# Kernel optimization log

Measured on AMD Instinct MI355X. Metric: run time of the kernel, lower is better.

The kernel has to match this reference:

```python
import jax, jax.numpy as jnp
import numpy as np

N_NODES = 16000
N_EDGES = 256000
F = 128        # invariant edge feature dim
MUL = 64       # multiplicity of env/V irreps (mul_gcd)
HID = 128      # mlp_n_hidden
SQRT3 = float(np.sqrt(3.0))

# e3nn-style activation normalization constant for silu:
# c = sqrt(E_{z~N(0,1)}[silu(z)^2]), so silu(z)/c has unit second moment.
_z = np.linspace(-12.0, 12.0, 100001)
_pdf = np.exp(-0.5 * _z ** 2) / np.sqrt(2.0 * np.pi)
_silu = _z / (1.0 + np.exp(-_z))
SILU_C = float(np.sqrt(np.trapz(_silu ** 2 * _pdf, _z)))


def _nsilu(x):
    return jax.nn.silu(x) / SILU_C


def _lin(x, W):
    # e3nn 'path' gradient normalization: W ~ N(0,1), forward scaled by 1/sqrt(fan_in)
    return (x @ W) / jnp.sqrt(jnp.asarray(W.shape[0], x.dtype))


def setup_inputs() -> dict:
    key = jax.random.key(0)
    ks = jax.random.split(key, 11)
    inp = {
        'vectors': jax.random.normal(ks[0], (N_EDGES, 3), jnp.float32),
        'x': jax.random.normal(ks[1], (N_EDGES, F), jnp.float32),
        'V': jax.random.normal(ks[2], (N_EDGES, 4 * MUL), jnp.float32),  # 64x0e + 64x1o
        'u': jax.random.uniform(ks[3], (N_EDGES,), jnp.float32),
        'm': jnp.ones((N_EDGES,), jnp.float32),
        'W_env': jax.random.normal(ks[4], (F, 2 * MUL), jnp.float32),
        'W1': jax.random.normal(ks[5], (F + 2 * MUL, HID), jnp.float32),
        'W2': jax.random.normal(ks[6], (HID, HID), jnp.float32),
        'W3': jax.random.normal(ks[7], (HID, HID), jnp.float32),
        'W_out': jax.random.normal(ks[8], (2 * MUL, MUL), jnp.float32),
        'senders': jax.random.randint(ks[9], (N_EDGES,), 0, N_NODES, jnp.int32),
    }
    return inp


def reference(vectors, x, V, u, m, W_env, W1, W2, W3, W_out, senders):
    E = vectors.shape[0]
    x = x * m[:, None]

    # n_neighbors = scatter_sum(m, dst=senders, map_back=True)
    n_neighbors = jax.ops.segment_sum(m, senders, num_segments=N_NODES)[senders]  # (E,)

    # w = Linear(num_irreps=2*MUL)(x)
    w = _lin(x, W_env)                  # (E, 128)
    w0, w1 = w[:, :MUL], w[:, MUL:]     # scalar / vector channel weights

    # spherical harmonics (component normalization): Y0 = 1, Y1 = sqrt(3)*rhat
    rhat = vectors / jnp.linalg.norm(vectors, axis=-1, keepdims=True)
    Y1 = SQRT3 * rhat                   # (E, 3)

    # w * Y * m, scatter_sum over senders, map back, normalize by n_neighbors
    denom = n_neighbors + 1e-5
    ws = w0 * m[:, None]                                   # (E, MUL)   w * Y0
    wv = (w1[:, :, None] * Y1[:, None, :]) * m[:, None, None]  # (E, MUL, 3)
    wY_s = jax.ops.segment_sum(ws, senders, num_segments=N_NODES)[senders] / denom[:, None]
    wY_v = jax.ops.segment_sum(wv, senders, num_segments=N_NODES)[senders] / denom[:, None, None]

    # V.mul_to_axis(): (E, MUL, 0e+1o)
    Vs = V[:, :MUL]                      # (E, MUL)
    Vv = V[:, MUL:].reshape(E, MUL, 3)   # (E, MUL, 3)

    # tensor product, filter_ir_out = {0e, 1o} (CG, component normalization)
    s_a = wY_s * Vs                                  # 0e x 0e -> 0e
    s_b = jnp.sum(wY_v * Vv, axis=-1) / SQRT3        # 1o x 1o -> 0e
    v_a = wY_s[:, :, None] * Vv                      # 0e x 1o -> 1o
    v_b = wY_v * Vs[:, :, None]                      # 1o x 0e -> 1o

    # scalars -> concatenated into x; vectors stay equivariant
    x = jnp.concatenate([x, s_a, s_b], axis=1)       # (E, F + 2*MUL)

    # invariant MLP (silu, no output activation)
    h = _nsilu(_lin(x, W1))
    h = _nsilu(_lin(h, W2))
    h = _lin(h, W3)                                  # (E, HID)
    x_out = u[:, None] * h

    # Linear(irreps_out=64x1o) on 128x1o
    V_in = jnp.concatenate([v_a, v_b], axis=1)       # (E, 2*MUL, 3)
    V_out = jnp.einsum('euk,uo->eok', V_in, W_out) / jnp.sqrt(jnp.asarray(2 * MUL, V.dtype))
    V_out = V_out.reshape(E, MUL * 3)                # (E, 192)

    return x_out, V_out
```

## Files before the change

### kernel.cpp

```cpp
#include <hip/hip_runtime.h>
#include <math.h>

typedef short bf16x8 __attribute__((ext_vector_type(8)));
typedef float f32x4 __attribute__((ext_vector_type(4)));

#define S128 0.08838834764831845f
#define S256I 0.0625f
#define NN_NODES 16000

#define WS_COUNTS   16448000
#define WS_OFFSETS  (WS_COUNTS + 64000)
#define WS_CURSOR   (WS_OFFSETS + 64000)
#define WS_INV      (WS_CURSOR + 64000)
#define WS_W1 (WS_INV + 1024000)
#define WS_W2 (WS_W1 + 65536)
#define WS_W3 (WS_W2 + 32768)
#define WS_WO (WS_W3 + 32768)
#define WS_WE (WS_WO + 16384)
#define WS_VECM (WS_WE + 32768)
#define WS_XMB  (WS_VECM + 4096000)

static float compute_inv_silu_c() {
    double sum = 0.0, prev = 0.0;
    const double dz = 24.0 / 100000.0;
    for (int i = 0; i <= 100000; ++i) {
        double z = -12.0 + dz * (double)i;
        double pdf = exp(-0.5 * z * z) * 0.3989422804014327;
        double s = z / (1.0 + exp(-z));
        double f = s * s * pdf;
        if (i) sum += 0.5 * (prev + f) * dz;
        prev = f;
    }
    return (float)(1.0 / sqrt(sum));
}
static const float INV_SILU_C = compute_inv_silu_c();

__device__ __forceinline__ unsigned int packbf(float a, float b) {
    union { float f; unsigned int u; } ca, cb;
    ca.f = a; cb.f = b;
    unsigned int ua = ca.u + (0x7fffu + ((ca.u >> 16) & 1u));
    unsigned int ub = cb.u + (0x7fffu + ((cb.u >> 16) & 1u));
    return (ua >> 16) | (ub & 0xffff0000u);
}
__device__ __forceinline__ unsigned short bf16r(float v) {
    union { float f; unsigned int u; } c; c.f = v;
    return (unsigned short)((c.u + (0x7fffu + ((c.u >> 16) & 1u))) >> 16);
}
__device__ __forceinline__ float bflo(unsigned int u) { return __uint_as_float(u << 16); }
__device__ __forceinline__ float bfhi(unsigned int u) { return __uint_as_float(u & 0xffff0000u); }
__device__ __forceinline__ int swz(int row, int b) { return b ^ ((row & 7) << 4); }
__device__ __forceinline__ float nsilu(float v, float ic) {
    return v / (1.0f + __expf(-v)) * ic;
}

__global__ __launch_bounds__(256) void k_wprep(
    const float* __restrict__ W1, const float* __restrict__ W2,
    const float* __restrict__ W3, const float* __restrict__ Wout,
    const float* __restrict__ Wenv, char* __restrict__ wsb)
{
    const int t = blockIdx.x * 256 + threadIdx.x;
    if (t < NN_NODES) ((int*)(wsb + WS_COUNTS))[t] = 0;
    if (t < 32768) {
        int n = t & 127, k = t >> 7;
        *(unsigned short*)(wsb + WS_W1 + n * 512 + k * 2) =
            bf16r(W1[k * 128 + n] * S256I);
    }
    if (t < 16384) {
        int n = t & 127, k = t >> 7;
        *(unsigned short*)(wsb + WS_W2 + n * 256 + k * 2) =
            bf16r(W2[k * 128 + n] * S128);
        *(unsigned short*)(wsb + WS_W3 + n * 256 + k * 2) =
            bf16r(W3[k * 128 + n] * S128);
    }
    if (t < 16384) {
        int j = t & 127, k = t >> 7;
        int c = (j & 1) ? 64 + (j >> 1) : (j >> 1);
        *(unsigned short*)(wsb + WS_WE + j * 256 + k * 2) =
            bf16r(Wenv[k * 128 + c] * S128);
    }
    if (t < 8192) {
        int o = t & 63, uu = t >> 6;
        *(unsigned short*)(wsb + WS_WO + o * 256 + ((uu * 2) ^ ((o & 7) << 4))) =
            bf16r(Wout[uu * 64 + o] * S128);
    }
}

__global__ __launch_bounds__(1024) void k_hist(
    const int* __restrict__ senders, int* __restrict__ counts, int E)
{
    const int e = blockIdx.x * 1024 + threadIdx.x;
    if (e < E) atomicAdd(&counts[senders[e]], 1);
}

__global__ __launch_bounds__(1024) void k_scan(
    const int* __restrict__ counts, int* __restrict__ offsets,
    int* __restrict__ cursor)
{
    __shared__ int part[1024];
    const int t = threadIdx.x;
    const int s0 = t * 16;
    const int s1 = (s0 + 16 < NN_NODES) ? s0 + 16 : NN_NODES;
    int s = 0;
    for (int i = s0; i < s1; ++i) s += counts[i];
    part[t] = s;
    __syncthreads();
    for (int off = 1; off < 1024; off <<= 1) {
        int v = part[t];
        if (t >= off) v += part[t - off];
        __syncthreads();
        part[t] = v;
        __syncthreads();
    }
    int run = t ? part[t - 1] : 0;
    for (int i = s0; i < s1; ++i) {
        offsets[i] = run; cursor[i] = run; run += counts[i];
    }
}

__global__ __launch_bounds__(1024) void k_binfill(
    const int* __restrict__ senders, const float* __restrict__ vectors,
    const float* __restrict__ m, int* __restrict__ cursor,
    int* __restrict__ inv, float4* __restrict__ vecm, int E)
{
    const int e = blockIdx.x * 1024 + threadIdx.x;
    if (e < E) {
        const int p = atomicAdd(&cursor[senders[e]], 1);
        inv[e] = p;
        float4 vm;
        vm.x = vectors[(size_t)e * 3 + 0];
        vm.y = vectors[(size_t)e * 3 + 1];
        vm.z = vectors[(size_t)e * 3 + 2];
        vm.w = m[e];
        vecm[p] = vm;
    }
}

__global__ __launch_bounds__(512) void k_env(
    const float* __restrict__ x, const float* __restrict__ m,
    const char* __restrict__ wsb, const int* __restrict__ inv,
    char* __restrict__ wout, char* __restrict__ xmb, int E)
{
    __shared__ char lds[32768];
    const int tid = threadIdx.x, l = tid & 63, wid = tid >> 6;
    const int lr = l & 15, lg = l >> 4;
    const int n0 = wid * 16;

    bf16x8 B[4];
    #pragma unroll
    for (int kk = 0; kk < 4; ++kk)
        B[kk] = *(const bf16x8*)(wsb + WS_WE + (n0 + lr) * 256 + kk * 64 + lg * 16);

    const int eb = blockIdx.x * 128;
    {
        const int el = tid >> 2, q = tid & 3;
        const int e = eb + el;
        if (e < E) {
            const float mv = m[e];
            const float4* xp = (const float4*)&x[(size_t)e * 128 + q * 32];
            #pragma unroll
            for (int j = 0; j < 4; ++j) {
                float4 A = xp[2 * j], Bv = xp[2 * j + 1];
                int4 w;
                w.x = packbf(A.x * mv, A.y * mv); w.y = packbf(A.z * mv, A.w * mv);
                w.z = packbf(Bv.x * mv, Bv.y * mv); w.w = packbf(Bv.z * mv, Bv.w * mv);
                *(int4*)(lds + el * 256 + swz(el, q * 64 + j * 16)) = w;
            }
        } else {
            const int4 z = {0, 0, 0, 0};
            #pragma unroll
            for (int j = 0; j < 4; ++j)
                *(int4*)(lds + el * 256 + swz(el, q * 64 + j * 16)) = z;
        }
    }
    __syncthreads();

    {
        const int el = tid >> 2, q = tid & 3;
        const int e = eb + el;
        if (e < E) {
            int4* d = (int4*)(xmb + (size_t)e * 256 + q * 64);
            #pragma unroll
            for (int j = 0; j < 4; ++j)
                d[j] = *(int4*)(lds + el * 256 + ((q * 64 + j * 16) ^ ((el & 7) << 4)));
        }
    }

    f32x4 acc[8];
    #pragma unroll
    for (int a = 0; a < 8; ++a) acc[a] = (f32x4){0.f, 0.f, 0.f, 0.f};

    #pragma unroll
    for (int kk = 0; kk < 4; ++kk) {
        const int kb = kk * 64 + lg * 16;
        #pragma unroll
        for (int mt = 0; mt < 8; ++mt) {
            const int row = mt * 16 + lr;
            bf16x8 a = *(const bf16x8*)(lds + row * 256 + swz(row, kb));
            acc[mt] = __builtin_amdgcn_mfma_f32_16x16x32_bf16(a, B[kk], acc[mt], 0, 0, 0);
        }
    }
    __syncthreads();

    #pragma unroll
    for (int mt = 0; mt < 8; ++mt)
        #pragma unroll
        for (int r = 0; r < 4; ++r) {
            const int row = mt * 16 + lg * 4 + r;
            *(unsigned short*)(lds + row * 256 + (((n0 + lr) * 2) ^ ((row & 7) << 4))) =
                bf16r(acc[mt][r]);
        }
    __syncthreads();

    {
        const int el = tid >> 2, q = tid & 3;
        const int e = eb + el;
        if (e < E) {
            const int p = inv[e];
            int4* d = (int4*)(wout + (size_t)p * 256 + q * 64);
            #pragma unroll
            for (int j = 0; j < 4; ++j)
                d[j] = *(int4*)(lds + el * 256 + ((q * 64 + j * 16) ^ ((el & 7) << 4)));
        }
    }
}

__global__ __launch_bounds__(256) void k_gather(
    const char* __restrict__ wvb, const float4* __restrict__ vecm,
    const int* __restrict__ counts, const int* __restrict__ offsets,
    float* __restrict__ node_cnt, float* __restrict__ node_s,
    float* __restrict__ node_v)
{
    const int l = threadIdx.x & 63, wid = threadIdx.x >> 6;
    const int n = blockIdx.x * 4 + wid;
    if (n >= NN_NODES) return;
    const int cnt = counts[n], base = offsets[n];

    float as = 0.f, a0 = 0.f, a1 = 0.f, a2 = 0.f, am = 0.f;
    for (int i = 0; i < cnt; ++i) {
        const unsigned int wv =
            *(const unsigned int*)(wvb + (size_t)(base + i) * 256 + l * 4);
        const float4 vm = vecm[base + i];
        const float rn = 1.7320508075688772f /
                         sqrtf(vm.x * vm.x + vm.y * vm.y + vm.z * vm.z);
        const float w0 = bflo(wv) * vm.w;
        const float c1 = bfhi(wv) * vm.w * rn;
        as += w0; am += vm.w;
        a0 += c1 * vm.x; a1 += c1 * vm.y; a2 += c1 * vm.z;
    }
    if (l == 0) node_cnt[n] = am;
    node_s[(size_t)n * 64 + l] = as;
    float* nv = &node_v[((size_t)n * 64 + l) * 3];
    nv[0] = a0; nv[1] = a1; nv[2] = a2;
}

__global__ __launch_bounds__(512, 4) void k_fuse(
    const float* __restrict__ V, const int* __restrict__ senders,
    const float* __restrict__ node_cnt, const float* __restrict__ node_s,
    const float* __restrict__ node_v, const char* __restrict__ wsb,
    const char* __restrict__ xmb, const float* __restrict__ ug,
    float* __restrict__ out_x, float* __restrict__ out_v,
    float inv_c, int E)
{
    __shared__ char lds[81920];
    const int tid = threadIdx.x, l = tid & 63, wid = tid >> 6;
    const int lr = l & 15, lg = l >> 4;

    {
        const int4* src = (const int4*)(wsb + WS_WO);
        ((int4*)(lds + 49152))[tid * 2]     = src[tid * 2];
        ((int4*)(lds + 49152))[tid * 2 + 1] = src[tid * 2 + 1];
    }

    const int eb = blockIdx.x * 64;
    #pragma unroll 2
    for (int i = 0; i < 8; ++i) {
        const int el = wid * 8 + i;
        const int e  = eb + el;
        float Vs = 0.f, Vv0 = 0.f, Vv1 = 0.f, Vv2 = 0.f;
        float wYs = 0.f, wv0 = 0.f, wv1 = 0.f, wv2 = 0.f;
        if (e < E) {
            Vs = V[(size_t)e * 256 + l];
            const float* vp = &V[(size_t)e * 256 + 64 + l * 3];
            Vv0 = vp[0]; Vv1 = vp[1]; Vv2 = vp[2];
            const int sn = senders[e];
            const float rden = 1.0f / (node_cnt[sn] + 1e-5f);
            wYs = node_s[(size_t)sn * 64 + l] * rden;
            const float* nvp = &node_v[((size_t)sn * 64 + l) * 3];
            wv0 = nvp[0] * rden; wv1 = nvp[1] * rden; wv2 = nvp[2] * rden;
        }
        *(unsigned short*)(lds + 65536 + el * 256 + l * 2) = bf16r(wYs * Vs);
        *(unsigned short*)(lds + 65536 + el * 256 + 128 + l * 2) =
            bf16r((wv0 * Vv0 + wv1 * Vv1 + wv2 * Vv2) * 0.57735026918962576f);
        const float vvk[3] = {Vv0, Vv1, Vv2};
        const float wvk[3] = {wv0, wv1, wv2};
        #pragma unroll
        for (int k = 0; k < 3; ++k) {
            const int row = el * 3 + k;
            *(unsigned short*)(lds + row * 256 + swz(row, l * 2))       = bf16r(wYs * vvk[k]);
            *(unsigned short*)(lds + row * 256 + swz(row, 128 + l * 2)) = bf16r(wvk[k] * Vs);
        }
    }
    __syncthreads();

    {
        const int wm = wid & 3, wn = wid >> 2;
        const int m0 = wm * 48, n0v = wn * 32;
        f32x4 acc[3][2];
        #pragma unroll
        for (int a = 0; a < 3; ++a)
            #pragma unroll
            for (int b = 0; b < 2; ++b) acc[a][b] = (f32x4){0.f, 0.f, 0.f, 0.f};

        #pragma unroll
        for (int kk = 0; kk < 4; ++kk) {
            const int kb = kk * 64 + lg * 16;
            bf16x8 a0 = *(const bf16x8*)(lds + (m0 + lr) * 256      + swz(m0 + lr, kb));
            bf16x8 a1 = *(const bf16x8*)(lds + (m0 + 16 + lr) * 256 + swz(m0 + 16 + lr, kb));
            bf16x8 a2 = *(const bf16x8*)(lds + (m0 + 32 + lr) * 256 + swz(m0 + 32 + lr, kb));
            bf16x8 b0 = *(const bf16x8*)(lds + 49152 + (n0v + lr) * 256      + swz(n0v + lr, kb));
            bf16x8 b1 = *(const bf16x8*)(lds + 49152 + (n0v + 16 + lr) * 256 + swz(n0v + 16 + lr, kb));
            acc[0][0] = __builtin_amdgcn_mfma_f32_16x16x32_bf16(a0, b0, acc[0][0], 0, 0, 0);
            acc[0][1] = __builtin_amdgcn_mfma_f32_16x16x32_bf16(a0, b1, acc[0][1], 0, 0, 0);
            acc[1][0] = __builtin_amdgcn_mfma_f32_16x16x32_bf16(a1, b0, acc[1][0], 0, 0, 0);
            acc[1][1] = __builtin_amdgcn_mfma_f32_16x16x32_bf16(a1, b1, acc[1][1], 0, 0, 0);
            acc[2][0] = __builtin_amdgcn_mfma_f32_16x16x32_bf16(a2, b0, acc[2][0], 0, 0, 0);
            acc[2][1] = __builtin_amdgcn_mfma_f32_16x16x32_bf16(a2, b1, acc[2][1], 0, 0, 0);
        }
        __syncthreads();

        #pragma unroll
        for (int mt = 0; mt < 3; ++mt)
            #pragma unroll
            for (int nt = 0; nt < 2; ++nt)
                #pragma unroll
                for (int r = 0; r < 4; ++r) {
                    const int mm = m0 + mt * 16 + lg * 4 + r;
                    const int el2 = mm / 3, kd = mm - el2 * 3;
                    const int o = n0v + nt * 16 + lr;
                    *(float*)(lds + el2 * 768 + (o * 3 + kd) * 4) = acc[mt][nt][r];
                }
    }
    __syncthreads();
    if (eb + 64 <= E) {
        const int4* s = (const int4*)lds;
        int4* d = (int4*)(out_v + (size_t)eb * 192);
        #pragma unroll
        for (int j = 0; j < 6; ++j) d[tid * 6 + j] = s[tid * 6 + j];
    } else {
        for (int idx = tid; idx < 64 * 192; idx += 512) {
            const int el2 = idx / 192;
            if (eb + el2 < E)
                out_v[(size_t)(eb + el2) * 192 + (idx % 192)] = *(float*)(lds + idx * 4);
        }
    }
    __syncthreads();

    const int n0 = wid * 16;
    bf16x8 B1[8];
    #pragma unroll
    for (int kk = 0; kk < 8; ++kk)
        B1[kk] = *(const bf16x8*)(wsb + WS_W1 + (n0 + lr) * 512 + kk * 64 + lg * 16);

    {
        const int el = tid >> 3, q = tid & 7;
        const int e = eb + el;
        int4 x0, x1;
        if (e < E) {
            const int4* xp = (const int4*)(xmb + (size_t)e * 256 + q * 32);
            x0 = xp[0]; x1 = xp[1];
        } else {
            x0 = (int4){0, 0, 0, 0}; x1 = (int4){0, 0, 0, 0};
        }
        *(int4*)(lds + el * 512 + swz(el, q * 32))      = x0;
        *(int4*)(lds + el * 512 + swz(el, q * 32 + 16)) = x1;
        int4 s0 = *(int4*)(lds + 65536 + el * 256 + q * 32);
        int4 s1 = *(int4*)(lds + 65536 + el * 256 + q * 32 + 16);
        *(int4*)(lds + el * 512 + swz(el, 256 + q * 32))      = s0;
        *(int4*)(lds + el * 512 + swz(el, 256 + q * 32 + 16)) = s1;
    }
    __syncthreads();

    f32x4 a1[4];
    #pragma unroll
    for (int a = 0; a < 4; ++a) a1[a] = (f32x4){0.f, 0.f, 0.f, 0.f};
    #pragma unroll
    for (int kk = 0; kk < 8; ++kk) {
        const int kb = kk * 64 + lg * 16;
        #pragma unroll
        for (int mt = 0; mt < 4; ++mt) {
            const int row = mt * 16 + lr;
            bf16x8 a = *(const bf16x8*)(lds + row * 512 + swz(row, kb));
            a1[mt] = __builtin_amdgcn_mfma_f32_16x16x32_bf16(a, B1[kk], a1[mt], 0, 0, 0);
        }
    }

    bf16x8 B2[4], B3[4];
    #pragma unroll
    for (int kk = 0; kk < 4; ++kk) {
        B2[kk] = *(const bf16x8*)(wsb + WS_W2 + (n0 + lr) * 256 + kk * 64 + lg * 16);
        B3[kk] = *(const bf16x8*)(wsb + WS_W3 + (n0 + lr) * 256 + kk * 64 + lg * 16);
    }

    #pragma unroll
    for (int mt = 0; mt < 4; ++mt)
        #pragma unroll
        for (int r = 0; r < 4; ++r) {
            const int row = mt * 16 + lg * 4 + r;
            *(unsigned short*)(lds + 32768 + row * 256 + swz(row, (n0 + lr) * 2)) =
                bf16r(nsilu(a1[mt][r], inv_c));
        }
    __syncthreads();

    f32x4 a2[4];
    #pragma unroll
    for (int a = 0; a < 4; ++a) a2[a] = (f32x4){0.f, 0.f, 0.f, 0.f};
    #pragma unroll
    for (int kk = 0; kk < 4; ++kk) {
        const int kb = kk * 64 + lg * 16;
        #pragma unroll
        for (int mt = 0; mt < 4; ++mt) {
            const int row = mt * 16 + lr;
            bf16x8 a = *(const bf16x8*)(lds + 32768 + row * 256 + swz(row, kb));
            a2[mt] = __builtin_amdgcn_mfma_f32_16x16x32_bf16(a, B2[kk], a2[mt], 0, 0, 0);
        }
    }
    #pragma unroll
    for (int mt = 0; mt < 4; ++mt)
        #pragma unroll
        for (int r = 0; r < 4; ++r) {
            const int row = mt * 16 + lg * 4 + r;
            *(unsigned short*)(lds + row * 256 + swz(row, (n0 + lr) * 2)) =
                bf16r(nsilu(a2[mt][r], inv_c));
        }
    __syncthreads();

    f32x4 a3[4];
    #pragma unroll
    for (int a = 0; a < 4; ++a) a3[a] = (f32x4){0.f, 0.f, 0.f, 0.f};
    #pragma unroll
    for (int kk = 0; kk < 4; ++kk) {
        const int kb = kk * 64 + lg * 16;
        #pragma unroll
        for (int mt = 0; mt < 4; ++mt) {
            const int row = mt * 16 + lr;
            bf16x8 a = *(const bf16x8*)(lds + row * 256 + swz(row, kb));
            a3[mt] = __builtin_amdgcn_mfma_f32_16x16x32_bf16(a, B3[kk], a3[mt], 0, 0, 0);
        }
    }
    __syncthreads();

    #pragma unroll
    for (int mt = 0; mt < 4; ++mt)
        #pragma unroll
        for (int r = 0; r < 4; ++r) {
            const int row = mt * 16 + lg * 4 + r;
            *(float*)(lds + row * 512 + (((n0 + lr) * 4) ^ ((row & 7) << 4))) = a3[mt][r];
        }
    __syncthreads();

    {
        const int el = tid >> 3, q = tid & 7;
        const int e = eb + el;
        if (e < E) {
            const float uu = ug[e];
            #pragma unroll
            for (int j = 0; j < 4; ++j) {
                int4 v = *(int4*)(lds + el * 512 + ((q * 64 + j * 16) ^ ((el & 7) << 4)));
                float4 f;
                f.x = __int_as_float(v.x) * uu; f.y = __int_as_float(v.y) * uu;
                f.z = __int_as_float(v.z) * uu; f.w = __int_as_float(v.w) * uu;
                *(float4*)(&out_x[(size_t)e * 128 + q * 16 + j * 4]) = f;
            }
        }
    }
}

extern "C" void kernel_launch(void* const* d_in, const int* in_sizes, int n_in,
                              void* d_out, int out_size, void* d_ws, size_t ws_size,
                              hipStream_t stream) {
    const float* vectors = (const float*)d_in[0];
    const float* x       = (const float*)d_in[1];
    const float* V       = (const float*)d_in[2];
    const float* u       = (const float*)d_in[3];
    const float* m       = (const float*)d_in[4];
    const float* W_env   = (const float*)d_in[5];
    const float* W1      = (const float*)d_in[6];
    const float* W2      = (const float*)d_in[7];
    const float* W3      = (const float*)d_in[8];
    const float* W_out   = (const float*)d_in[9];
    const int*   senders = (const int*)d_in[10];

    const int E = in_sizes[4];

    char*  wsb      = (char*)d_ws;
    float* node_cnt = (float*)d_ws;
    float* node_s   = node_cnt + NN_NODES;
    float* node_v   = node_s + (size_t)NN_NODES * 64;
    int* counts  = (int*)(wsb + WS_COUNTS);
    int* offsets = (int*)(wsb + WS_OFFSETS);
    int* cursor  = (int*)(wsb + WS_CURSOR);
    int* inv     = (int*)(wsb + WS_INV);
    float4* vecm = (float4*)(wsb + WS_VECM);
    char* xmb    = wsb + WS_XMB;

    float* out_x = (float*)d_out;
    float* out_v = out_x + (size_t)E * 128;
    char*  wvb   = (char*)out_v;

    k_wprep<<<128, 256, 0, stream>>>(W1, W2, W3, W_out, W_env, wsb);
    k_hist<<<(E + 1023) / 1024, 1024, 0, stream>>>(senders, counts, E);
    k_scan<<<1, 1024, 0, stream>>>(counts, offsets, cursor);
    k_binfill<<<(E + 1023) / 1024, 1024, 0, stream>>>(senders, vectors, m,
                                                      cursor, inv, vecm, E);
    k_env<<<(E + 127) / 128, 512, 0, stream>>>(x, m, wsb, inv, wvb, xmb, E);
    k_gather<<<(NN_NODES + 3) / 4, 256, 0, stream>>>(wvb, vecm, counts, offsets,
                                                     node_cnt, node_s, node_v);
    k_fuse<<<(E + 63) / 64, 512, 0, stream>>>(V, senders, node_cnt, node_s,
                                              node_v, wsb, xmb, u,
                                              out_x, out_v, INV_SILU_C, E);
}
```

Before: 439.8 us.

## Shrink k_fuse LDS footprint to raise occupancy, keep W_out in registers

```diff
diff --git a/kernel.cpp b/kernel.cpp
--- a/kernel.cpp
+++ b/kernel.cpp
@@ -48,7 +48,7 @@
 }
 __device__ __forceinline__ float bflo(unsigned int u) { return __uint_as_float(u << 16); }
 __device__ __forceinline__ float bfhi(unsigned int u) { return __uint_as_float(u & 0xffff0000u); }
-__device__ __forceinline__ int swz(int row, int b) { return b ^ ((row & 7) << 4); }
+__device__ __forceinline__ int swz(int row, int b) { return b ^ ((row & 15) << 4); }
 __device__ __forceinline__ float nsilu(float v, float ic) {
     return v / (1.0f + __expf(-v)) * ic;
 }
@@ -80,7 +80,7 @@
     }
     if (t < 8192) {
         int o = t & 63, uu = t >> 6;
-        *(unsigned short*)(wsb + WS_WO + o * 256 + ((uu * 2) ^ ((o & 7) << 4))) =
+        *(unsigned short*)(wsb + WS_WO + o * 256 + uu * 2) =
             bf16r(Wout[uu * 64 + o] * S128);
     }
 }
@@ -181,7 +181,7 @@
             int4* d = (int4*)(xmb + (size_t)e * 256 + q * 64);
             #pragma unroll
             for (int j = 0; j < 4; ++j)
-                d[j] = *(int4*)(lds + el * 256 + ((q * 64 + j * 16) ^ ((el & 7) << 4)));
+                d[j] = *(int4*)(lds + el * 256 + swz(el, q * 64 + j * 16));
         }
     }
 
@@ -206,7 +206,7 @@
         #pragma unroll
         for (int r = 0; r < 4; ++r) {
             const int row = mt * 16 + lg * 4 + r;
-            *(unsigned short*)(lds + row * 256 + (((n0 + lr) * 2) ^ ((row & 7) << 4))) =
+            *(unsigned short*)(lds + row * 256 + swz(row, (n0 + lr) * 2)) =
                 bf16r(acc[mt][r]);
         }
     __syncthreads();
@@ -219,7 +219,7 @@
             int4* d = (int4*)(wout + (size_t)p * 256 + q * 64);
             #pragma unroll
             for (int j = 0; j < 4; ++j)
-                d[j] = *(int4*)(lds + el * 256 + ((q * 64 + j * 16) ^ ((el & 7) << 4)));
+                d[j] = *(int4*)(lds + el * 256 + swz(el, q * 64 + j * 16));
         }
     }
 }
@@ -253,7 +253,7 @@
     nv[0] = a0; nv[1] = a1; nv[2] = a2;
 }
 
-__global__ __launch_bounds__(512, 4) void k_fuse(
+__global__ __launch_bounds__(512, 6) void k_fuse(
     const float* __restrict__ V, const int* __restrict__ senders,
     const float* __restrict__ node_cnt, const float* __restrict__ node_s,
     const float* __restrict__ node_v, const char* __restrict__ wsb,
@@ -261,18 +261,13 @@
     float* __restrict__ out_x, float* __restrict__ out_v,
     float inv_c, int E)
 {
-    __shared__ char lds[81920];
+    __shared__ char lds[49152];
     const int tid = threadIdx.x, l = tid & 63, wid = tid >> 6;
     const int lr = l & 15, lg = l >> 4;
-
-    {
-        const int4* src = (const int4*)(wsb + WS_WO);
-        ((int4*)(lds + 49152))[tid * 2]     = src[tid * 2];
-        ((int4*)(lds + 49152))[tid * 2 + 1] = src[tid * 2 + 1];
-    }
-
     const int eb = blockIdx.x * 64;
-    #pragma unroll 2
+
+    unsigned int sab[8];
+    #pragma unroll
     for (int i = 0; i < 8; ++i) {
         const int el = wid * 8 + i;
         const int e  = eb + el;
@@ -288,9 +283,8 @@
             const float* nvp = &node_v[((size_t)sn * 64 + l) * 3];
             wv0 = nvp[0] * rden; wv1 = nvp[1] * rden; wv2 = nvp[2] * rden;
         }
-        *(unsigned short*)(lds + 65536 + el * 256 + l * 2) = bf16r(wYs * Vs);
-        *(unsigned short*)(lds + 65536 + el * 256 + 128 + l * 2) =
-            bf16r((wv0 * Vv0 + wv1 * Vv1 + wv2 * Vv2) * 0.57735026918962576f);
+        sab[i] = packbf(wYs * Vs,
+                        (wv0 * Vv0 + wv1 * Vv1 + wv2 * Vv2) * 0.57735026918962576f);
         const float vvk[3] = {Vv0, Vv1, Vv2};
         const float wvk[3] = {wv0, wv1, wv2};
         #pragma unroll
@@ -300,11 +294,18 @@
             *(unsigned short*)(lds + row * 256 + swz(row, 128 + l * 2)) = bf16r(wvk[k] * Vs);
         }
     }
-    __syncthreads();
-
-    {
-        const int wm = wid & 3, wn = wid >> 2;
-        const int m0 = wm * 48, n0v = wn * 32;
+
+    const int wm = wid & 3, wn = wid >> 2;
+    const int m0 = wm * 48, n0v = wn * 32;
+    bf16x8 Bo0[4], Bo1[4];
+    #pragma unroll
+    for (int kk = 0; kk < 4; ++kk) {
+        Bo0[kk] = *(const bf16x8*)(wsb + WS_WO + (n0v + lr) * 256      + kk * 64 + lg * 16);
+        Bo1[kk] = *(const bf16x8*)(wsb + WS_WO + (n0v + 16 + lr) * 256 + kk * 64 + lg * 16);
+    }
+    __syncthreads();
+
+    {
         f32x4 acc[3][2];
         #pragma unroll
         for (int a = 0; a < 3; ++a)
@@ -317,14 +318,12 @@
             bf16x8 a0 = *(const bf16x8*)(lds + (m0 + lr) * 256      + swz(m0 + lr, kb));
             bf16x8 a1 = *(const bf16x8*)(lds + (m0 + 16 + lr) * 256 + swz(m0 + 16 + lr, kb));
             bf16x8 a2 = *(const bf16x8*)(lds + (m0 + 32 + lr) * 256 + swz(m0 + 32 + lr, kb));
-            bf16x8 b0 = *(const bf16x8*)(lds + 49152 + (n0v + lr) * 256      + swz(n0v + lr, kb));
-            bf16x8 b1 = *(const bf16x8*)(lds + 49152 + (n0v + 16 + lr) * 256 + swz(n0v + 16 + lr, kb));
-            acc[0][0] = __builtin_amdgcn_mfma_f32_16x16x32_bf16(a0, b0, acc[0][0], 0, 0, 0);
-            acc[0][1] = __builtin_amdgcn_mfma_f32_16x16x32_bf16(a0, b1, acc[0][1], 0, 0, 0);
-            acc[1][0] = __builtin_amdgcn_mfma_f32_16x16x32_bf16(a1, b0, acc[1][0], 0, 0, 0);
-            acc[1][1] = __builtin_amdgcn_mfma_f32_16x16x32_bf16(a1, b1, acc[1][1], 0, 0, 0);
-            acc[2][0] = __builtin_amdgcn_mfma_f32_16x16x32_bf16(a2, b0, acc[2][0], 0, 0, 0);
-            acc[2][1] = __builtin_amdgcn_mfma_f32_16x16x32_bf16(a2, b1, acc[2][1], 0, 0, 0);
+            acc[0][0] = __builtin_amdgcn_mfma_f32_16x16x32_bf16(a0, Bo0[kk], acc[0][0], 0, 0, 0);
+            acc[0][1] = __builtin_amdgcn_mfma_f32_16x16x32_bf16(a0, Bo1[kk], acc[0][1], 0, 0, 0);
+            acc[1][0] = __builtin_amdgcn_mfma_f32_16x16x32_bf16(a1, Bo0[kk], acc[1][0], 0, 0, 0);
+            acc[1][1] = __builtin_amdgcn_mfma_f32_16x16x32_bf16(a1, Bo1[kk], acc[1][1], 0, 0, 0);
+            acc[2][0] = __builtin_amdgcn_mfma_f32_16x16x32_bf16(a2, Bo0[kk], acc[2][0], 0, 0, 0);
+            acc[2][1] = __builtin_amdgcn_mfma_f32_16x16x32_bf16(a2, Bo1[kk], acc[2][1], 0, 0, 0);
         }
         __syncthreads();
 
@@ -371,12 +370,18 @@
         } else {
             x0 = (int4){0, 0, 0, 0}; x1 = (int4){0, 0, 0, 0};
         }
-        *(int4*)(lds + el * 512 + swz(el, q * 32))      = x0;
-        *(int4*)(lds + el * 512 + swz(el, q * 32 + 16)) = x1;
-        int4 s0 = *(int4*)(lds + 65536 + el * 256 + q * 32);
-        int4 s1 = *(int4*)(lds + 65536 + el * 256 + q * 32 + 16);
-        *(int4*)(lds + el * 512 + swz(el, 256 + q * 32))      = s0;
-        *(int4*)(lds + el * 512 + swz(el, 256 + q * 32 + 16)) = s1;
+        *(int4*)(lds + el * 256 + swz(el, q * 32))      = x0;
+        *(int4*)(lds + el * 256 + swz(el, q * 32 + 16)) = x1;
+    }
+    {
+        #pragma unroll
+        for (int i = 0; i < 8; ++i) {
+            const int el = wid * 8 + i;
+            *(unsigned short*)(lds + 16384 + el * 256 + swz(el, l * 2)) =
+                (unsigned short)(sab[i] & 0xffffu);
+            *(unsigned short*)(lds + 16384 + el * 256 + swz(el, 128 + l * 2)) =
+                (unsigned short)(sab[i] >> 16);
+        }
     }
     __syncthreads();
 
@@ -385,11 +390,12 @@
     for (int a = 0; a < 4; ++a) a1[a] = (f32x4){0.f, 0.f, 0.f, 0.f};
     #pragma unroll
     for (int kk = 0; kk < 8; ++kk) {
-        const int kb = kk * 64 + lg * 16;
+        const int base = (kk < 4) ? 0 : 16384;
+        const int kb = (kk & 3) * 64 + lg * 16;
         #pragma unroll
         for (int mt = 0; mt < 4; ++mt) {
             const int row = mt * 16 + lr;
-            bf16x8 a = *(const bf16x8*)(lds + row * 512 + swz(row, kb));
+            bf16x8 a = *(const bf16x8*)(lds + base + row * 256 + swz(row, kb));
             a1[mt] = __builtin_amdgcn_mfma_f32_16x16x32_bf16(a, B1[kk], a1[mt], 0, 0, 0);
         }
     }
@@ -449,13 +455,17 @@
     }
     __syncthreads();
 
-    #pragma unroll
-    for (int mt = 0; mt < 4; ++mt)
-        #pragma unroll
-        for (int r = 0; r < 4; ++r) {
-            const int row = mt * 16 + lg * 4 + r;
-            *(float*)(lds + row * 512 + (((n0 + lr) * 4) ^ ((row & 7) << 4))) = a3[mt][r];
-        }
+    {
+        const int base = (n0 < 64) ? 0 : 16384;
+        const int colb = (n0 & 63) + 0;
+        #pragma unroll
+        for (int mt = 0; mt < 4; ++mt)
+            #pragma unroll
+            for (int r = 0; r < 4; ++r) {
+                const int row = mt * 16 + lg * 4 + r;
+                *(float*)(lds + base + row * 256 + swz(row, (colb + lr) * 4)) = a3[mt][r];
+            }
+    }
     __syncthreads();
 
     {
@@ -465,7 +475,9 @@
             const float uu = ug[e];
             #pragma unroll
             for (int j = 0; j < 4; ++j) {
-                int4 v = *(int4*)(lds + el * 512 + ((q * 64 + j * 16) ^ ((el & 7) << 4)));
+                const int b = q * 64 + j * 16;
+                const int base = (b < 256) ? 0 : 16384;
+                int4 v = *(int4*)(lds + base + el * 256 + swz(el, b & 255));
                 float4 f;
                 f.x = __int_as_float(v.x) * uu; f.y = __int_as_float(v.y) * uu;
                 f.z = __int_as_float(v.z) * uu; f.w = __int_as_float(v.w) * uu;
```

After: 692.0 us. 1.57x slower.
